# Kernel tuning notes

Measured on AMD Instinct MI355X. Metric: run time of the kernel, lower is better.

Reference implementation:

```python
import jax, jax.numpy as jnp
import numpy as np

N, E, IN, HID, HEADS, K = 50000, 800000, 7, 64, 4, 4


def _add_self_loops(src, dst, edge_attr, n):
    # PyG add_self_loops with fill_value='mean': loop attr = mean of incoming edge attrs per node
    ones = jnp.ones((src.shape[0],), edge_attr.dtype)
    cnt = jax.ops.segment_sum(ones, dst, num_segments=n)
    loop_attr = jax.ops.segment_sum(edge_attr, dst, num_segments=n) / jnp.maximum(cnt, 1.0)[:, None]
    ar = jnp.arange(n, dtype=src.dtype)
    return (jnp.concatenate([src, ar]), jnp.concatenate([dst, ar]),
            jnp.concatenate([edge_attr, loop_attr], axis=0))


def _gat_conv(x, src, dst, eattr, W, a_src, a_dst, We, a_edge, bias, heads, outc, concat, n):
    xw = (x @ W).reshape(n, heads, outc)                      # [N,H,C]
    al_s = jnp.sum(xw * a_src, -1)                            # [N,H]
    al_d = jnpm if False else jnp.sum(xw * a_dst, -1)         # [N,H]
    ew = (eattr @ We).reshape(-1, heads, outc)                # [E,H,C]
    al_e = jnp.sum(ew * a_edge, -1)                           # [E,H]
    alpha = jax.nn.leaky_relu(al_s[src] + al_d[dst] + al_e, 0.2)
    # segment softmax over incoming edges of each dst node (every node has a self loop)
    m = jax.ops.segment_max(alpha, dst, num_segments=n)
    alpha = jnp.exp(alpha - m[dst])
    denom = jax.ops.segment_sum(alpha, dst, num_segments=n)
    alpha = alpha / (denom[dst] + 1e-16)
    out = jax.ops.segment_sum(xw[src] * alpha[..., None], dst, num_segments=n)  # [N,H,C]
    out = out.reshape(n, heads * outc) if concat else out.mean(axis=1)
    return out + bias


def setup_inputs() -> dict:
    key = jax.random.key(0)
    ks = jax.random.split(key, 24)
    s = lambda d: 1.0 / np.sqrt(d)
    inp = {
        'x': jax.random.uniform(ks[0], (N, IN), jnp.float32),
        'edge_index': jax.random.randint(ks[1], (2, E), 0, N),
        'edge_attr': jax.random.uniform(ks[2], (E, 1), jnp.float32),
        'assignments': jax.random.randint(ks[3], (N,), 0, K),
        # conv1 (heads=4, concat)
        'W1': jax.random.normal(ks[4], (IN, HEADS * HID), jnp.float32) * s(IN),
        'att_src1': jax.random.normal(ks[5], (HEADS, HID), jnp.float32) * s(HID),
        'att_dst1': jax.random.normal(ks[6], (HEADS, HID), jnp.float32) * s(HID),
        'We1': jax.random.normal(ks[7], (1, HEADS * HID), jnp.float32),
        'att_e1': jax.random.normal(ks[8], (HEADS, HID), jnp.float32) * s(HID),
        'b1': jnp.zeros((HEADS * HID,), jnp.float32),
        # conv2 (heads=1, mean)
        'W2': jax.random.normal(ks[9], (HEADS * HID, HID), jnp.float32) * s(HEADS * HID),
        'att_src2': jax.random.normal(ks[10], (1, HID), jnp.float32) * s(HID),
        'att_dst2': jax.random.normal(ks[11], (1, HID), jnp.float32) * s(HID),
        'We2': jax.random.normal(ks[12], (1, HID), jnp.float32),
        'att_e2': jax.random.normal(ks[13], (1, HID), jnp.float32) * s(HID),
        'b2': jnp.zeros((HID,), jnp.float32),
        # actor MLP: Linear(HID+1, HID) -> ReLU -> Linear(HID, 1)
        'A1': jax.random.normal(ks[14], (HID + 1, HID), jnp.float32) * s(HID + 1),
        'c1': jnp.zeros((HID,), jnp.float32),
        'A2': jax.random.normal(ks[15], (HID, 1), jnp.float32) * s(HID),
        'c2': jnp.zeros((1,), jnp.float32),
    }
    return inp


def reference(x, edge_index, edge_attr, assignments,
              W1, att_src1, att_dst1, We1, att_e1, b1,
              W2, att_src2, att_dst2, We2, att_e2, b2,
              A1, c1, A2, c2):
    n = x.shape[0]
    src, dst, ea = _add_self_loops(edge_index[0], edge_index[1], edge_attr, n)
    h = jax.nn.elu(_gat_conv(x, src, dst, ea, W1, att_src1, att_dst1, We1, att_e1, b1,
                             HEADS, HID, True, n))
    h = _gat_conv(h, src, dst, ea, W2, att_src2, att_dst2, We2, att_e2, b2,
                  1, HID, False, n)
    # masked segment-mean pooling over clusters (all K clusters non-empty w.h.p.)
    ones = jnp.ones((n,), h.dtype)
    cnt = jax.ops.segment_sum(ones, assignments, num_segments=K)
    safe = jnp.maximum(cnt, 1.0)
    z = jax.ops.segment_sum(h, assignments, num_segments=K) / safe[:, None]     # [K,HID]
    cf = jax.ops.segment_sum(x[:, 6], assignments, num_segments=K) / safe       # [K]
    nonempty = (cnt > 0)
    z = jnp.where(nonempty[:, None], z, 0.0)
    cf = jnp.where(nonempty, cf, 0.0)
    zcf = jnp.concatenate([z, cf[:, None]], axis=-1)                            # [K,HID+1]
    logits = (jax.nn.relu(zcf @ A1 + c1) @ A2 + c2)[:, 0]                        # [K]
    probs = jax.nn.softmax(logits)[None, :]                                      # [1,K]
    z_flat = z.reshape(1, -1)                                                    # [1,K*HID]
    return probs, z_flat
```

## Files before the change

### kernel.cpp

```cpp
#include <hip/hip_runtime.h>
#include <hip/hip_bf16.h>

#define HEADS 4
#define KCL 4
#define BSHIFT 5
#define BW 32
#define NBUCKMAX 1568
#define BCAP 1024
#define EPT 8
typedef unsigned long long u64;
typedef short short8 __attribute__((ext_vector_type(8)));
typedef float f32x4 __attribute__((ext_vector_type(4)));

__device__ __forceinline__ unsigned short bf16_rne(float f) {
    unsigned int u = __float_as_uint(f);
    u += 0x7FFFu + ((u >> 16) & 1u);
    return (unsigned short)(u >> 16);
}
__device__ __forceinline__ float bf16_to_f32(unsigned short h) {
    return __uint_as_float(((unsigned int)h) << 16);
}


__global__ __launch_bounds__(256) void k_prep_bin(const float* __restrict__ x,
                                                  const float* __restrict__ W1, const float* __restrict__ W2,
                                                  const float* __restrict__ as1, const float* __restrict__ ad1,
                                                  const float* __restrict__ as2, const float* __restrict__ ad2,
                                                  const float* __restrict__ We1, const float* __restrict__ ae1,
                                                  const float* __restrict__ We2, const float* __restrict__ ae2,
                                                  float* __restrict__ ce1, float* __restrict__ ce2,
                                                  float* __restrict__ u_s, float* __restrict__ u_d,
                                                  unsigned short* __restrict__ W2T,
                                                  float* __restrict__ nrec,
                                                  const int* __restrict__ src, const int* __restrict__ dst,
                                                  const float* __restrict__ ea,
                                                  unsigned int* __restrict__ gtail,
                                                  u64* __restrict__ gbuck,
                                                  int N_, int E_, int NB, int nbuck) {
    int t = threadIdx.x;
    if ((int)blockIdx.x >= NB) {
        __shared__ unsigned int cnt[NBUCKMAX];
        __shared__ unsigned int gb[NBUCKMAX];
        for (int i = t; i < nbuck; i += 256) cnt[i] = 0u;
        __syncthreads();
        int bid = blockIdx.x - NB;
        int e0 = bid * (256 * EPT) + t;
        u64 pk[EPT]; int bk[EPT]; unsigned int ls[EPT];
#pragma unroll
        for (int i = 0; i < EPT; i++) {
            int e = e0 + i * 256;
            bool valid = e < E_;
            int s = 0, d = 0; float a = 0.0f;
            if (valid) { s = src[e]; d = dst[e]; a = ea[e]; }
            int b = d >> BSHIFT;
            int lo = d & (BW - 1);
            pk[i] = ((u64)__float_as_uint(a) << 32) | ((u64)(unsigned int)lo << 24) | (unsigned int)s;
            bk[i] = b;
            ls[i] = valid ? atomicAdd(&cnt[b], 1u) : 0u;
        }
        __syncthreads();
        for (int i = t; i < nbuck; i += 256)
            gb[i] = (cnt[i] > 0u) ? atomicAdd(&gtail[i], cnt[i]) : 0u;
        __syncthreads();
#pragma unroll
        for (int i = 0; i < EPT; i++) {
            if (e0 + i * 256 < E_) {
                unsigned int pos = gb[bk[i]] + ls[i];
                if (pos < BCAP) gbuck[(size_t)bk[i] * BCAP + pos] = pk[i];
            }
        }
        return;
    }
    __shared__ float Ps_l[7][4], Pd_l[7][4];
    int h = t >> 6, lane = t & 63;
    for (int i = 0; i < 7; i++) {
        float a = W1[i * 256 + t];
        float ps = a * as1[t];
        float pd = a * ad1[t];
        for (int off = 32; off; off >>= 1) {
            ps += __shfl_down(ps, off, 64);
            pd += __shfl_down(pd, off, 64);
        }
        if (lane == 0) { Ps_l[i][h] = ps; Pd_l[i][h] = pd; }
    }
    if (blockIdx.x == 0) {
        float p = We1[t] * ae1[t];
        for (int off = 32; off; off >>= 1) p += __shfl_down(p, off, 64);
        if (lane == 0) ce1[h] = p;
        if (t < 64) {
            float q = We2[t] * ae2[t];
            for (int off = 32; off; off >>= 1) q += __shfl_down(q, off, 64);
            if (t == 0) ce2[0] = q;
        }
        float us = 0.f, ud = 0.f;
        const float* wr = W2 + t * 64;
        for (int n = 0; n < 64; n++) { us += wr[n] * as2[n]; ud += wr[n] * ad2[n]; }
        u_s[t] = us; u_d[t] = ud;
    }
    int gidx = blockIdx.x * 256 + t;
    if (gidx < 16384) {
        int nn = gidx & 63, k = gidx >> 6;
        W2T[nn * 256 + k] = bf16_rne(W2[k * 64 + nn]);
    }
    __syncthreads();
    int n = gidx;
    if (n >= N_) return;
    float xv[7];
#pragma unroll
    for (int i = 0; i < 7; i++) xv[i] = x[n * 7 + i];
    float4 als = make_float4(0.f, 0.f, 0.f, 0.f);
    float4 ald = make_float4(0.f, 0.f, 0.f, 0.f);
#pragma unroll
    for (int i = 0; i < 7; i++) {
        als.x += xv[i] * Ps_l[i][0]; als.y += xv[i] * Ps_l[i][1];
        als.z += xv[i] * Ps_l[i][2]; als.w += xv[i] * Ps_l[i][3];
        ald.x += xv[i] * Pd_l[i][0]; ald.y += xv[i] * Pd_l[i][1];
        ald.z += xv[i] * Pd_l[i][2]; ald.w += xv[i] * Pd_l[i][3];
    }
    float4* nr = (float4*)(nrec + (size_t)n * 16);
    nr[0] = als;
    nr[1] = ald;
    nr[2] = make_float4(xv[0], xv[1], xv[2], xv[3]);
    nr[3] = make_float4(xv[4], xv[5], xv[6], 0.0f);
}

__global__ __launch_bounds__(256) void k_agg1_xw2g(const unsigned int* __restrict__ gtail,
                                                   const u64* __restrict__ gbuck,
                                                   u64* __restrict__ gpacked,
                                                   int2* __restrict__ idx2,
                                                   const float* __restrict__ nrec,
                                                   const float* __restrict__ ce1,
                                                   const float* __restrict__ W1,
                                                   const float* __restrict__ b1,
                                                   const unsigned short* __restrict__ W2T,
                                                   const float* __restrict__ u_s,
                                                   const float* __restrict__ u_d,
                                                   unsigned short* __restrict__ xw2b,
                                                   float* __restrict__ al_s2,
                                                   float* __restrict__ al_d2, int N_) {
    __shared__ float Xs2[32][36];
    __shared__ __align__(16) unsigned short A_lds[32][264];
    __shared__ u64 esorted[BCAP];
    __shared__ unsigned int rdeg[32], rstart[32], rcur[32];
    __shared__ float als_p[32], ald_p[32];
    int t = threadIdx.x;
    int b = blockIdx.x;
    int m0 = b * 32;
    size_t base = (size_t)b * BCAP;
    u64* raw = (u64*)&A_lds[0][0];
    unsigned int n = gtail[b]; if (n > BCAP) n = BCAP;
    if (t < 32) rdeg[t] = 0u;
    __syncthreads();
    for (unsigned int pos = t; pos < n; pos += 256) {
        u64 p = __builtin_nontemporal_load(&gbuck[base + pos]);
        raw[pos] = p;
        atomicAdd(&rdeg[(unsigned int)(p >> 24) & 31u], 1u);
    }
    __syncthreads();
    if (t < 32) {
        unsigned int deg = rdeg[t];
        unsigned int inc = deg;
#pragma unroll
        for (int off = 1; off < 32; off <<= 1) {
            unsigned int u = __shfl_up(inc, off, 64);
            if (t >= off) inc += u;
        }
        unsigned int start = inc - deg;
        rstart[t] = start; rcur[t] = start;
        if (m0 + t < N_) idx2[m0 + t] = make_int2((int)(base + start), (int)deg);
    }
    __syncthreads();
    for (unsigned int pos = t; pos < n; pos += 256) {
        u64 p = raw[pos];
        unsigned int slot = atomicAdd(&rcur[(unsigned int)(p >> 24) & 31u], 1u);
        esorted[slot] = p;
    }
    __syncthreads();
    for (unsigned int pos = t; pos < n; pos += 256) gpacked[base + pos] = esorted[pos];
    {
        int dl = t >> 3, d = m0 + dl;
        int sub = t & 7, h = sub >> 1, half = sub & 1;
        bool act = d < N_;
        float4 A = make_float4(0.f, 0.f, 0.f, 0.f);
        float4 B = make_float4(0.f, 0.f, 0.f, 0.f);
        if (act) {
            const u64* row = esorted + rstart[dl];
            int cnt = (int)rdeg[dl];
            const float* nd = nrec + (size_t)d * 16;
            float ald = nd[4 + h];
            float ce = ce1[h];
            float easum = 0.0f;
#define E1(J) { \
            u64 p = row[(J)]; \
            int s = (int)(p & 0xFFFFFFu); \
            float a = __uint_as_float((unsigned int)(p >> 32)); \
            const float* ns = nrec + (size_t)s * 16; \
            float als = ns[h]; \
            float4 xa = *(const float4*)(ns + 8); \
            float4 xb = *(const float4*)(ns + 12); \
            easum += a; \
            float v = als + ald + a * ce; \
            v = v > 0.f ? v : 0.2f * v; \
            float w = __expf(v); \
            A.x += w * xa.x; A.y += w * xa.y; A.z += w * xa.z; A.w += w * xa.w; \
            B.x += w * xb.x; B.y += w * xb.y; B.z += w * xb.z; B.w += w; }
            int j = half;
            for (; j + 6 < cnt; j += 8) { E1(j); E1(j + 2); E1(j + 4); E1(j + 6); }
            for (; j < cnt; j += 2) { E1(j); }
#undef E1
            A.x += __shfl_xor(A.x, 1, 64);
            A.y += __shfl_xor(A.y, 1, 64);
            A.z += __shfl_xor(A.z, 1, 64);
            A.w += __shfl_xor(A.w, 1, 64);
            B.x += __shfl_xor(B.x, 1, 64);
            B.y += __shfl_xor(B.y, 1, 64);
            B.z += __shfl_xor(B.z, 1, 64);
            B.w += __shfl_xor(B.w, 1, 64);
            easum += __shfl_xor(easum, 1, 64);
            if (!half) {
                float a_self = easum / fmaxf((float)cnt, 1.0f);
                float v = nd[h] + ald + a_self * ce;
                v = v > 0.f ? v : 0.2f * v;
                float w = __expf(v);
                float4 xa = *(const float4*)(nd + 8);
                float4 xb = *(const float4*)(nd + 12);
                A.x += w * xa.x; A.y += w * xa.y; A.z += w * xa.z; A.w += w * xa.w;
                B.x += w * xb.x; B.y += w * xb.y; B.z += w * xb.z; B.w += w;
            }
        }
        if (!half) {
            *(float4*)&Xs2[dl][h * 8] = A;
            *(float4*)&Xs2[dl][h * 8 + 4] = B;
        }
    }
    __syncthreads();
    {
        int r = t >> 3;
        int kk = t & 7;
        float ps = 0.f, pd = 0.f;
#pragma unroll
        for (int hh = 0; hh < 4; hh++) {
            float xv[7];
#pragma unroll
            for (int i = 0; i < 7; i++) xv[i] = Xs2[r][hh * 8 + i];
            float rw = 1.0f / (Xs2[r][hh * 8 + 7] + 1e-16f);
#pragma unroll
            for (int q = 0; q < 8; q++) {
                int k = hh * 64 + q * 8 + kk;
                float s = 0.f;
#pragma unroll
                for (int i = 0; i < 7; i++) s += xv[i] * W1[i * 256 + k];
                float v = s * rw + b1[k];
                float a = v > 0.f ? v : (__expf(v) - 1.0f);
                ps += a * u_s[k];
                pd += a * u_d[k];
                A_lds[r][k] = bf16_rne(a);
            }
        }
        ps += __shfl_xor(ps, 1, 64); pd += __shfl_xor(pd, 1, 64);
        ps += __shfl_xor(ps, 2, 64); pd += __shfl_xor(pd, 2, 64);
        ps += __shfl_xor(ps, 4, 64); pd += __shfl_xor(pd, 4, 64);
        if (kk == 0) { als_p[r] = ps; ald_p[r] = pd; }
    }
    __syncthreads();
    {
        int w = t >> 6, lane = t & 63;
        int mm = lane & 15, quad = lane >> 4;
        int n0 = w * 16;
        f32x4 acc0 = {0.f, 0.f, 0.f, 0.f};
        f32x4 acc1 = {0.f, 0.f, 0.f, 0.f};
        const unsigned short* bptr = W2T + (size_t)(n0 + mm) * 256;
#pragma unroll
        for (int step = 0; step < 8; step++) {
            int kf = step * 32 + quad * 8;
            short8 bf = *(const short8*)&bptr[kf];
            short8 af0 = *(const short8*)&A_lds[mm][kf];
            short8 af1 = *(const short8*)&A_lds[16 + mm][kf];
            acc0 = __builtin_amdgcn_mfma_f32_16x16x32_bf16(af0, bf, acc0, 0, 0, 0);
            acc1 = __builtin_amdgcn_mfma_f32_16x16x32_bf16(af1, bf, acc1, 0, 0, 0);
        }
#pragma unroll
        for (int r = 0; r < 4; r++) {
            int row0 = m0 + quad * 4 + r;
            if (row0 < N_) xw2b[(size_t)row0 * 64 + n0 + mm] = bf16_rne(acc0[r]);
            int row1 = row0 + 16;
            if (row1 < N_) xw2b[(size_t)row1 * 64 + n0 + mm] = bf16_rne(acc1[r]);
        }
    }
    if (t < 32 && m0 + t < N_) { al_s2[m0 + t] = als_p[t]; al_d2[m0 + t] = ald_p[t]; }
}

__global__ __launch_bounds__(256) void k_agg2f(const int2* __restrict__ idx2,
                                               const u64* __restrict__ gpacked,
                                               const float* __restrict__ al_s2,
                                               const float* __restrict__ al_d2,
                                               const float* __restrict__ ce2,
                                               const unsigned short* __restrict__ xw2b,
                                               float* __restrict__ h2, int N_) {
    int wid = threadIdx.x >> 6, lane = threadIdx.x & 63;
    int d = blockIdx.x * 4 + wid;
    if (d >= N_) return;
    int2 ix = idx2[d];
    const u64* row = gpacked + ix.x;
    int cnt = ix.y;
    float ald = al_d2[d];
    float ce = ce2[0];
    float acc = 0.0f;
    float wlane = 0.0f, alane = 0.0f;
    for (int pos = 0; pos < cnt; pos += 64) {
        int nle = min(64, cnt - pos);
        float w = 0.0f, a = 0.0f;
        int s = d;
        if (lane < nle) {
            u64 p = __builtin_nontemporal_load(&row[pos + lane]);
            s = (int)(p & 0xFFFFFFu);
            a = __uint_as_float((unsigned int)(p >> 32));
            float v = al_s2[s] + ald + a * ce;
            v = v > 0.f ? v : 0.2f * v;
            w = __expf(v);
        }
        wlane += w;
        alane += a;
        int jj = 0;
#define G1(OFS) \
        float w##OFS = __uint_as_float(__builtin_amdgcn_readlane(__float_as_uint(w), jj + OFS)); \
        int   s##OFS = __builtin_amdgcn_readlane(s, jj + OFS);
        for (; jj + 7 < nle; jj += 8) {
            G1(0) G1(1) G1(2) G1(3) G1(4) G1(5) G1(6) G1(7)
            acc += w0 * bf16_to_f32(xw2b[(size_t)s0 * 64 + lane])
                 + w1 * bf16_to_f32(xw2b[(size_t)s1 * 64 + lane])
                 + w2 * bf16_to_f32(xw2b[(size_t)s2 * 64 + lane])
                 + w3 * bf16_to_f32(xw2b[(size_t)s3 * 64 + lane])
                 + w4 * bf16_to_f32(xw2b[(size_t)s4 * 64 + lane])
                 + w5 * bf16_to_f32(xw2b[(size_t)s5 * 64 + lane])
                 + w6 * bf16_to_f32(xw2b[(size_t)s6 * 64 + lane])
                 + w7 * bf16_to_f32(xw2b[(size_t)s7 * 64 + lane]);
        }
        for (; jj < nle; jj++) {
            G1(0)
            acc += w0 * bf16_to_f32(xw2b[(size_t)s0 * 64 + lane]);
        }
#undef G1
    }
    float wsum = wlane, easum = alane;
    for (int off = 32; off; off >>= 1) {
        wsum += __shfl_xor(wsum, off, 64);
        easum += __shfl_xor(easum, off, 64);
    }
    float a_self = easum / fmaxf((float)cnt, 1.0f);
    float v = al_s2[d] + ald + a_self * ce;
    v = v > 0.f ? v : 0.2f * v;
    float w = __expf(v);
    acc += w * bf16_to_f32(xw2b[(size_t)d * 64 + lane]);
    wsum += w;
    h2[(size_t)d * 64 + lane] = acc / (wsum + 1e-16f);
}

__global__ __launch_bounds__(256) void k_pool(const float* __restrict__ h2, const float* __restrict__ x,
                                              const int* __restrict__ assign,
                                              float* __restrict__ zsum, float* __restrict__ cntK,
                                              float* __restrict__ cfK, int nNodes) {
    __shared__ float lz[KCL * 64];
    __shared__ float lc[KCL];
    __shared__ float lf[KCL];
    int t = threadIdx.x;
    lz[t] = 0.0f;
    if (t < KCL) { lc[t] = 0.0f; lf[t] = 0.0f; }
    __syncthreads();
    int lane = t & 63, wid = t >> 6;
    for (int n = blockIdx.x * 4 + wid; n < nNodes; n += gridDim.x * 4) {
        int a = assign[n];
        atomicAdd(&lz[a * 64 + lane], h2[(size_t)n * 64 + lane]);
        if (lane == 0) {
            atomicAdd(&lc[a], 1.0f);
            atomicAdd(&lf[a], x[n * 7 + 6]);
        }
    }
    __syncthreads();
    atomicAdd(&zsum[t], lz[t]);
    if (t < KCL) {
        atomicAdd(&cntK[t], lc[t]);
        atomicAdd(&cfK[t], lf[t]);
    }
}

__global__ __launch_bounds__(256) void k_head(const float* __restrict__ zsum, const float* __restrict__ cntK,
                                              const float* __restrict__ cfK, const float* __restrict__ b2,
                                              const float* __restrict__ A1, const float* __restrict__ c1,
                                              const float* __restrict__ A2, const float* __restrict__ c2,
                                              float* __restrict__ out) {
    __shared__ float zcf[KCL][65];
    __shared__ float logits[KCL];
    int t = threadIdx.x;
    int k = t >> 6, c = t & 63;
    float cn = cntK[k];
    float z = (cn > 0.f) ? (zsum[k * 64 + c] / fmaxf(cn, 1.0f) + b2[c]) : 0.0f;
    zcf[k][c] = z;
    out[4 + k * 64 + c] = z;
    if (c == 0) zcf[k][64] = (cn > 0.f) ? (cfK[k] / fmaxf(cn, 1.0f)) : 0.0f;
    __syncthreads();
    {
        int j = c;
        float acc = 0.0f;
        for (int i = 0; i < 65; i++) acc += zcf[k][i] * A1[i * 64 + j];
        float hr = fmaxf(acc + c1[j], 0.0f);
        float contrib = hr * A2[j];
        for (int off = 32; off; off >>= 1) contrib += __shfl_down(contrib, off, 64);
        if (j == 0) logits[k] = contrib + c2[0];
    }
    __syncthreads();
    if (t == 0) {
        float m = fmaxf(fmaxf(logits[0], logits[1]), fmaxf(logits[2], logits[3]));
        float e0 = expf(logits[0] - m), e1 = expf(logits[1] - m);
        float e2 = expf(logits[2] - m), e3 = expf(logits[3] - m);
        float s = e0 + e1 + e2 + e3;
        out[0] = e0 / s; out[1] = e1 / s; out[2] = e2 / s; out[3] = e3 / s;
    }
}

extern "C" void kernel_launch(void* const* d_in, const int* in_sizes, int n_in,
                              void* d_out, int out_size, void* d_ws, size_t ws_size,
                              hipStream_t stream) {
    const float* x      = (const float*)d_in[0];
    const int*   ei     = (const int*)d_in[1];
    const float* eattr  = (const float*)d_in[2];
    const int*   assign = (const int*)d_in[3];
    const float* W1     = (const float*)d_in[4];
    const float* as1    = (const float*)d_in[5];
    const float* ad1    = (const float*)d_in[6];
    const float* We1    = (const float*)d_in[7];
    const float* ae1    = (const float*)d_in[8];
    const float* b1     = (const float*)d_in[9];
    const float* W2     = (const float*)d_in[10];
    const float* as2    = (const float*)d_in[11];
    const float* ad2    = (const float*)d_in[12];
    const float* We2    = (const float*)d_in[13];
    const float* ae2    = (const float*)d_in[14];
    const float* b2     = (const float*)d_in[15];
    const float* A1     = (const float*)d_in[16];
    const float* c1     = (const float*)d_in[17];
    const float* A2     = (const float*)d_in[18];
    const float* c2     = (const float*)d_in[19];
    float* out = (float*)d_out;

    const int N_ = in_sizes[0] / 7;
    const int E_ = in_sizes[2];
    const int NB = (N_ + 255) / 256;
    const int nbuck = (N_ + BW - 1) >> BSHIFT;
    const int NBBIN = (E_ + 256 * EPT - 1) / (256 * EPT);
    const int* srcA = ei;
    const int* dstA = ei + E_;

    float* ws = (float*)d_ws;
    size_t Nz = (size_t)N_;
    float* nrec    = ws;
    float* al_s2   = nrec + 16 * Nz;
    float* al_d2   = al_s2 + Nz;
    float* ce1     = al_d2 + Nz;
    float* ce2     = ce1 + 4;
    float* zsum    = ce2 + 4;
    float* cntK    = zsum + 256;
    float* cfK     = cntK + 4;
    unsigned int* gtail  = (unsigned int*)(cfK + 4);
    float* u_s     = (float*)(gtail + NBUCKMAX);
    float* u_d     = u_s + 256;
    unsigned short* xw2b = (unsigned short*)(u_d + 256);
    float* h2      = (float*)(xw2b + 64 * Nz);
    uintptr_t pp   = (uintptr_t)(h2 + 64 * Nz);
    u64* gbuck     = (u64*)((pp + 7) & ~(uintptr_t)7);
    u64* gpacked   = gbuck + (size_t)nbuck * BCAP;
    int2* idx2     = (int2*)(gpacked + (size_t)nbuck * BCAP);
    unsigned short* W2T = (unsigned short*)(idx2 + Nz);

    hipMemsetAsync(zsum, 0, (size_t)(264 + NBUCKMAX) * sizeof(float), stream);

    k_prep_bin<<<NB + NBBIN, 256, 0, stream>>>(x, W1, W2, as1, ad1, as2, ad2,
                                               We1, ae1, We2, ae2,
                                               ce1, ce2, u_s, u_d, W2T, nrec,
                                               srcA, dstA, eattr, gtail, gbuck,
                                               N_, E_, NB, nbuck);

    k_agg1_xw2g<<<nbuck, 256, 0, stream>>>(gtail, gbuck, gpacked, idx2, nrec, ce1,
                                           W1, b1, W2T, u_s, u_d,
                                           xw2b, al_s2, al_d2, N_);

    k_agg2f<<<(N_ + 3) / 4, 256, 0, stream>>>(idx2, gpacked, al_s2, al_d2, ce2, xw2b, h2, N_);
    k_pool<<<256, 256, 0, stream>>>(h2, x, assign, zsum, cntK, cfK, N_);

    k_head<<<1, 256, 0, stream>>>(zsum, cntK, cfK, b2, A1, c1, A2, c2, out);
}
```

Before: 233.3 us.

## Fuse layer-2 aggregation with cluster pooling using 8-lane-per-node gather

Merges the second GAT aggregation kernel with the pooling kernel so h2 is never written to or read back from global memory. It also remaps work from one wavefront per destination node to eight threads per node, each loading 16-byte bf16 vectors from the gathered rows, with edges processed two at a time. Pooled sums are accumulated into shared-memory atomics inside the same persistent grid of 512 blocks. The risks are imbalance across nodes from serial per-thread edge loops and contention on the shared atomics across only four clusters. The tile count is passed as nbuck, which assumes 32-node tiles match the bucket count.

```diff
diff --git a/kernel.cpp b/kernel.cpp
--- a/kernel.cpp
+++ b/kernel.cpp
@@ -290,90 +290,83 @@
     if (t < 32 && m0 + t < N_) { al_s2[m0 + t] = als_p[t]; al_d2[m0 + t] = ald_p[t]; }
 }
 
-__global__ __launch_bounds__(256) void k_agg2f(const int2* __restrict__ idx2,
+__global__ __launch_bounds__(256) void k_agg2p(const int2* __restrict__ idx2,
                                                const u64* __restrict__ gpacked,
                                                const float* __restrict__ al_s2,
                                                const float* __restrict__ al_d2,
                                                const float* __restrict__ ce2,
                                                const unsigned short* __restrict__ xw2b,
-                                               float* __restrict__ h2, int N_) {
-    int wid = threadIdx.x >> 6, lane = threadIdx.x & 63;
-    int d = blockIdx.x * 4 + wid;
-    if (d >= N_) return;
-    int2 ix = idx2[d];
-    const u64* row = gpacked + ix.x;
-    int cnt = ix.y;
-    float ald = al_d2[d];
-    float ce = ce2[0];
-    float acc = 0.0f;
-    float wlane = 0.0f, alane = 0.0f;
-    for (int pos = 0; pos < cnt; pos += 64) {
-        int nle = min(64, cnt - pos);
-        float w = 0.0f, a = 0.0f;
-        int s = d;
-        if (lane < nle) {
-            u64 p = __builtin_nontemporal_load(&row[pos + lane]);
-            s = (int)(p & 0xFFFFFFu);
-            a = __uint_as_float((unsigned int)(p >> 32));
-            float v = al_s2[s] + ald + a * ce;
-            v = v > 0.f ? v : 0.2f * v;
-            w = __expf(v);
-        }
-        wlane += w;
-        alane += a;
-        int jj = 0;
-#define G1(OFS) \
-        float w##OFS = __uint_as_float(__builtin_amdgcn_readlane(__float_as_uint(w), jj + OFS)); \
-        int   s##OFS = __builtin_amdgcn_readlane(s, jj + OFS);
-        for (; jj + 7 < nle; jj += 8) {
-            G1(0) G1(1) G1(2) G1(3) G1(4) G1(5) G1(6) G1(7)
-            acc += w0 * bf16_to_f32(xw2b[(size_t)s0 * 64 + lane])
-                 + w1 * bf16_to_f32(xw2b[(size_t)s1 * 64 + lane])
-                 + w2 * bf16_to_f32(xw2b[(size_t)s2 * 64 + lane])
-                 + w3 * bf16_to_f32(xw2b[(size_t)s3 * 64 + lane])
-                 + w4 * bf16_to_f32(xw2b[(size_t)s4 * 64 + lane])
-                 + w5 * bf16_to_f32(xw2b[(size_t)s5 * 64 + lane])
-                 + w6 * bf16_to_f32(xw2b[(size_t)s6 * 64 + lane])
-                 + w7 * bf16_to_f32(xw2b[(size_t)s7 * 64 + lane]);
-        }
-        for (; jj < nle; jj++) {
-            G1(0)
-            acc += w0 * bf16_to_f32(xw2b[(size_t)s0 * 64 + lane]);
-        }
-#undef G1
-    }
-    float wsum = wlane, easum = alane;
-    for (int off = 32; off; off >>= 1) {
-        wsum += __shfl_xor(wsum, off, 64);
-        easum += __shfl_xor(easum, off, 64);
-    }
-    float a_self = easum / fmaxf((float)cnt, 1.0f);
-    float v = al_s2[d] + ald + a_self * ce;
-    v = v > 0.f ? v : 0.2f * v;
-    float w = __expf(v);
-    acc += w * bf16_to_f32(xw2b[(size_t)d * 64 + lane]);
-    wsum += w;
-    h2[(size_t)d * 64 + lane] = acc / (wsum + 1e-16f);
-}
-
-__global__ __launch_bounds__(256) void k_pool(const float* __restrict__ h2, const float* __restrict__ x,
-                                              const int* __restrict__ assign,
-                                              float* __restrict__ zsum, float* __restrict__ cntK,
-                                              float* __restrict__ cfK, int nNodes) {
-    __shared__ float lz[KCL * 64];
-    __shared__ float lc[KCL];
-    __shared__ float lf[KCL];
+                                               const float* __restrict__ x,
+                                               const int* __restrict__ assign,
+                                               float* __restrict__ zsum, float* __restrict__ cntK,
+                                               float* __restrict__ cfK, int N_, int ntiles) {
+    __shared__ float lz[256];
+    __shared__ float lc[KCL], lf[KCL];
     int t = threadIdx.x;
     lz[t] = 0.0f;
     if (t < KCL) { lc[t] = 0.0f; lf[t] = 0.0f; }
     __syncthreads();
-    int lane = t & 63, wid = t >> 6;
-    for (int n = blockIdx.x * 4 + wid; n < nNodes; n += gridDim.x * 4) {
-        int a = assign[n];
-        atomicAdd(&lz[a * 64 + lane], h2[(size_t)n * 64 + lane]);
-        if (lane == 0) {
+    int dl = t >> 3, sub = t & 7;
+    float ce = ce2[0];
+    for (int tile = blockIdx.x; tile < ntiles; tile += gridDim.x) {
+        int d = tile * 32 + dl;
+        if (d >= N_) continue;
+        int2 ix = idx2[d];
+        const u64* row = gpacked + ix.x;
+        int cnt = ix.y;
+        float ald = al_d2[d];
+        float acc[8];
+#pragma unroll
+        for (int f = 0; f < 8; f++) acc[f] = 0.0f;
+        float wsum = 0.0f, easum = 0.0f;
+        const unsigned short* xcol = xw2b + sub * 8;
+        int j = 0;
+        for (; j + 1 < cnt; j += 2) {
+            u64 p0 = row[j], p1 = row[j + 1];
+            int s0 = (int)(p0 & 0xFFFFFFu), s1 = (int)(p1 & 0xFFFFFFu);
+            float a0 = __uint_as_float((unsigned int)(p0 >> 32));
+            float a1 = __uint_as_float((unsigned int)(p1 >> 32));
+            float als0 = al_s2[s0], als1 = al_s2[s1];
+            short8 g0 = *(const short8*)&xcol[(size_t)s0 * 64];
+            short8 g1 = *(const short8*)&xcol[(size_t)s1 * 64];
+            easum += a0 + a1;
+            float v0 = als0 + ald + a0 * ce; v0 = v0 > 0.f ? v0 : 0.2f * v0;
+            float v1 = als1 + ald + a1 * ce; v1 = v1 > 0.f ? v1 : 0.2f * v1;
+            float w0 = __expf(v0), w1 = __expf(v1);
+            wsum += w0 + w1;
+#pragma unroll
+            for (int f = 0; f < 8; f++)
+                acc[f] += w0 * bf16_to_f32((unsigned short)g0[f])
+                        + w1 * bf16_to_f32((unsigned short)g1[f]);
+        }
+        if (j < cnt) {
+            u64 p0 = row[j];
+            int s0 = (int)(p0 & 0xFFFFFFu);
+            float a0 = __uint_as_float((unsigned int)(p0 >> 32));
+            float als0 = al_s2[s0];
+            short8 g0 = *(const short8*)&xcol[(size_t)s0 * 64];
+            easum += a0;
+            float v0 = als0 + ald + a0 * ce; v0 = v0 > 0.f ? v0 : 0.2f * v0;
+            float w0 = __expf(v0);
+            wsum += w0;
+#pragma unroll
+            for (int f = 0; f < 8; f++) acc[f] += w0 * bf16_to_f32((unsigned short)g0[f]);
+        }
+        float a_self = easum / fmaxf((float)cnt, 1.0f);
+        float v = al_s2[d] + ald + a_self * ce;
+        v = v > 0.f ? v : 0.2f * v;
+        float w = __expf(v);
+        short8 gd = *(const short8*)&xcol[(size_t)d * 64];
+#pragma unroll
+        for (int f = 0; f < 8; f++) acc[f] += w * bf16_to_f32((unsigned short)gd[f]);
+        wsum += w;
+        float rw = 1.0f / (wsum + 1e-16f);
+        int a = assign[d];
+#pragma unroll
+        for (int f = 0; f < 8; f++) atomicAdd(&lz[a * 64 + sub * 8 + f], acc[f] * rw);
+        if (sub == 0) {
             atomicAdd(&lc[a], 1.0f);
-            atomicAdd(&lf[a], x[n * 7 + 6]);
+            atomicAdd(&lf[a], x[d * 7 + 6]);
         }
     }
     __syncthreads();
@@ -465,8 +458,7 @@
     float* u_s     = (float*)(gtail + NBUCKMAX);
     float* u_d     = u_s + 256;
     unsigned short* xw2b = (unsigned short*)(u_d + 256);
-    float* h2      = (float*)(xw2b + 64 * Nz);
-    uintptr_t pp   = (uintptr_t)(h2 + 64 * Nz);
+    uintptr_t pp   = (uintptr_t)(xw2b + 64 * Nz);
     u64* gbuck     = (u64*)((pp + 7) & ~(uintptr_t)7);
     u64* gpacked   = gbuck + (size_t)nbuck * BCAP;
     int2* idx2     = (int2*)(gpacked + (size_t)nbuck * BCAP);
@@ -484,8 +476,8 @@
                                            W1, b1, W2T, u_s, u_d,
                                            xw2b, al_s2, al_d2, N_);
 
-    k_agg2f<<<(N_ + 3) / 4, 256, 0, stream>>>(idx2, gpacked, al_s2, al_d2, ce2, xw2b, h2, N_);
-    k_pool<<<256, 256, 0, stream>>>(h2, x, assign, zsum, cntK, cfK, N_);
+    k_agg2p<<<512, 256, 0, stream>>>(idx2, gpacked, al_s2, al_d2, ce2, xw2b,
+                                     x, assign, zsum, cntK, cfK, N_, nbuck);
 
     k_head<<<1, 256, 0, stream>>>(zsum, cntK, cfK, b2, A1, c1, A2, c2, out);
 }
```

After: 219.8 us. -5.8%, faster.
